# Optimization experiments

Hardware: AMD Instinct MI355X
Metric: run time of the kernel (lower is better)

## Reference

```python
import jax, jax.numpy as jnp
import numpy as np

S, L, D = 50, 1024, 768
D4 = D // 4

def _ln(x, g, b, eps=1e-5):
    m = jnp.mean(x, axis=-1, keepdims=True)
    v = jnp.mean((x - m) ** 2, axis=-1, keepdims=True)
    return (x - m) * jax.lax.rsqrt(v + eps) * g + b

def _attn(x, Wq, Wk, Wv):
    # x: [N, D]; low-rank q/k (D4), values are the raw input, then output proj Wv.
    q = x @ Wq                      # [N, D4]
    k = x @ Wk                      # [N, D4]
    u = (q @ k.T) / jnp.sqrt(jnp.float32(q.shape[-1]))
    a = jax.nn.softmax(u, axis=-1)  # [N, N]
    return (a @ x) @ Wv             # [N, D]

def setup_inputs() -> dict:
    key = jax.random.key(0)
    ks = jax.random.split(key, 16)
    g = lambda i, shape: jax.random.normal(ks[i], shape, dtype=jnp.float32) * 0.02
    return dict(
        x=jax.random.normal(ks[0], (S, L, D), dtype=jnp.float32),
        pre_Wq=g(1, (S, D, D4)), pre_Wk=g(2, (S, D, D4)), pre_Wv=g(3, (S, D, D)),
        ln1_g=jnp.ones((S, D)), ln1_b=jnp.zeros((S, D)),
        pre_W1=g(4, (S, D, D4)), pre_b1=jnp.zeros((S, D4)),
        pre_W2=g(5, (S, D4, D)), pre_b2=jnp.zeros((S, D)),
        ln4p_g=jnp.ones((S, D)), ln4p_b=jnp.zeros((S, D)),
        cross_Wq=g(6, (D, D4)), cross_Wk=g(7, (D, D4)), cross_Wv=g(8, (D, D)),
        ln2_g=jnp.ones((D,)), ln2_b=jnp.zeros((D,)),
        post_Wq=g(9, (S, D, D4)), post_Wk=g(10, (S, D, D4)), post_Wv=g(11, (S, D, D)),
        ln3_g=jnp.ones((S, D)), ln3_b=jnp.zeros((S, D)),
        post_W1=g(12, (S, D, D4)), post_b1=jnp.zeros((S, D4)),
        post_W2=g(13, (S, D4, D)), post_b2=jnp.zeros((S, D)),
        ln4_g=jnp.ones((S, D)), ln4_b=jnp.zeros((S, D)),
    )

def reference(x, pre_Wq, pre_Wk, pre_Wv, ln1_g, ln1_b,
              pre_W1, pre_b1, pre_W2, pre_b2, ln4p_g, ln4p_b,
              cross_Wq, cross_Wk, cross_Wv, ln2_g, ln2_b,
              post_Wq, post_Wk, post_Wv, ln3_g, ln3_b,
              post_W1, post_b1, post_W2, post_b2, ln4_g, ln4_b):
    # step_wise forward; dropout is identity at inference.
    # pre_self_step: per-step Attention (step dim vmapped == loop over n_step)
    h = jax.vmap(_attn)(x, pre_Wq, pre_Wk, pre_Wv)          # [S, L, D]
    x = jax.vmap(_ln)(x + h, ln1_g, ln1_b)
    # pre_mlp: per-step bottleneck MLP
    h = jax.nn.relu(jnp.einsum('sld,sdf->slf', x, pre_W1) + pre_b1[:, None, :])
    h = jnp.einsum('slf,sfd->sld', h, pre_W2) + pre_b2[:, None, :]
    x = jax.vmap(_ln)(x + h, ln4p_g, ln4p_b)
    # cross_step: shared Attention over the step axis (seq positions as batch)
    xt = jnp.transpose(x, (1, 0, 2))                        # [L, S, D]
    h = jax.vmap(_attn, in_axes=(0, None, None, None))(xt, cross_Wq, cross_Wk, cross_Wv)
    xt = _ln(xt + h, ln2_g, ln2_b)
    x = jnp.transpose(xt, (1, 0, 2))                        # [S, L, D]
    # post_self_step
    h = jax.vmap(_attn)(x, post_Wq, post_Wk, post_Wv)
    x = jax.vmap(_ln)(x + h, ln3_g, ln3_b)
    # post_mlp
    h = jax.nn.relu(jnp.einsum('sld,sdf->slf', x, post_W1) + post_b1[:, None, :])
    h = jnp.einsum('slf,sfd->sld', h, post_W2) + post_b2[:, None, :]
    x = jax.vmap(_ln)(x + h, ln4_g, ln4_b)
    return x
```

## Files before the change

### kernel.cpp

```cpp
#include <hip/hip_runtime.h>


typedef __bf16 bf16x8 __attribute__((ext_vector_type(8)));
typedef float f32x4 __attribute__((ext_vector_type(4)));

template<int BNN, int BF32>
__global__ __launch_bounds__(256) void gemm_k(
    const __bf16* __restrict__ A, const void* __restrict__ Bv, __bf16* __restrict__ C,
    int M, int N, int K, int Kb,
    int lda, int ldb, int ldc,
    long long sA, long long sB, long long sC,
    const float* __restrict__ bias, long long sBias, int relu)
{
    __shared__ __bf16 As[64][72];
    __shared__ __bf16 Bs[64][72];

    const int batch = blockIdx.z;
    A += (long long)batch * sA;
    C += (long long)batch * sC;

    const int m0 = blockIdx.x * 64;
    const int n0 = blockIdx.y * 64;
    const int tid = threadIdx.x;
    const int lane = tid & 63;
    const int wave = tid >> 6;
    const int wr = wave >> 1, wc = wave & 1;

    f32x4 acc[2][2];
    #pragma unroll
    for (int i = 0; i < 2; i++)
        #pragma unroll
        for (int j = 0; j < 2; j++)
            acc[i][j] = f32x4{0.f, 0.f, 0.f, 0.f};

    for (int kb = 0; kb < K; kb += 64) {
        {
            const int row = tid >> 2;
            const int cs = (tid & 3) << 4;
            const int gr = m0 + row;
            __bf16* dst = &As[row][cs];
            if (gr < M) {
                const __bf16* src = A + (long long)gr * lda + kb + cs;
                *(bf16x8*)dst       = *(const bf16x8*)src;
                *(bf16x8*)(dst + 8) = *(const bf16x8*)(src + 8);
            } else {
                #pragma unroll
                for (int i = 0; i < 16; i++) dst[i] = (__bf16)0.f;
            }
        }
        if (BNN) {
            const int kk = tid >> 2;
            const int ns = (tid & 3) << 4;
            const int gk = kb + kk;
            const bool kok = gk < Kb;
            if (BF32) {
                const float* src = (const float*)Bv + (long long)batch * sB
                                 + (long long)gk * ldb + n0 + ns;
                if (kok && (n0 + ns + 16 <= N)) {
                    #pragma unroll
                    for (int q = 0; q < 4; q++) {
                        float4 v = *(const float4*)(src + 4 * q);
                        Bs[ns + 4 * q + 0][kk] = (__bf16)v.x;
                        Bs[ns + 4 * q + 1][kk] = (__bf16)v.y;
                        Bs[ns + 4 * q + 2][kk] = (__bf16)v.z;
                        Bs[ns + 4 * q + 3][kk] = (__bf16)v.w;
                    }
                } else {
                    for (int i = 0; i < 16; i++) {
                        const int n = n0 + ns + i;
                        Bs[ns + i][kk] = (kok && n < N) ? (__bf16)src[i] : (__bf16)0.f;
                    }
                }
            } else {
                const __bf16* src = (const __bf16*)Bv + (long long)batch * sB
                                  + (long long)gk * ldb + n0 + ns;
                if (kok && (n0 + ns + 16 <= N)) {
                    bf16x8 v0 = *(const bf16x8*)src;
                    bf16x8 v1 = *(const bf16x8*)(src + 8);
                    #pragma unroll
                    for (int i = 0; i < 8; i++) Bs[ns + i][kk] = v0[i];
                    #pragma unroll
                    for (int i = 0; i < 8; i++) Bs[ns + 8 + i][kk] = v1[i];
                } else {
                    for (int i = 0; i < 16; i++) {
                        const int n = n0 + ns + i;
                        Bs[ns + i][kk] = (kok && n < N) ? src[i] : (__bf16)0.f;
                    }
                }
            }
        } else {
            const int row = tid >> 2;
            const int cs = (tid & 3) << 4;
            const int gn = n0 + row;
            __bf16* dst = &Bs[row][cs];
            if (gn < N) {
                const __bf16* src = (const __bf16*)Bv + (long long)batch * sB
                                  + (long long)gn * ldb + kb + cs;
                *(bf16x8*)dst       = *(const bf16x8*)src;
                *(bf16x8*)(dst + 8) = *(const bf16x8*)(src + 8);
            } else {
                #pragma unroll
                for (int i = 0; i < 16; i++) dst[i] = (__bf16)0.f;
            }
        }
        __syncthreads();

        #pragma unroll
        for (int ks = 0; ks < 64; ks += 32) {
            const int kf = ks + ((lane >> 4) << 3);
            bf16x8 av[2], bv[2];
            #pragma unroll
            for (int mi = 0; mi < 2; mi++)
                av[mi] = *(const bf16x8*)&As[wr * 32 + mi * 16 + (lane & 15)][kf];
            #pragma unroll
            for (int ni = 0; ni < 2; ni++)
                bv[ni] = *(const bf16x8*)&Bs[wc * 32 + ni * 16 + (lane & 15)][kf];
            #pragma unroll
            for (int mi = 0; mi < 2; mi++)
                #pragma unroll
                for (int ni = 0; ni < 2; ni++)
                    acc[mi][ni] = __builtin_amdgcn_mfma_f32_16x16x32_bf16(
                        av[mi], bv[ni], acc[mi][ni], 0, 0, 0);
        }
        __syncthreads();
    }

    const int rb = (lane >> 4) << 2;
    const int cc = lane & 15;
    #pragma unroll
    for (int mi = 0; mi < 2; mi++) {
        #pragma unroll
        for (int ni = 0; ni < 2; ni++) {
            const int col = n0 + wc * 32 + ni * 16 + cc;
            if (col >= N) continue;
            float bvl = 0.f;
            if (bias) bvl = bias[(long long)batch * sBias + col];
            #pragma unroll
            for (int r = 0; r < 4; r++) {
                const int row = m0 + wr * 32 + mi * 16 + rb + r;
                if (row < M) {
                    float v = acc[mi][ni][r] + bvl;
                    if (relu) v = fmaxf(v, 0.f);
                    C[(long long)row * ldc + col] = (__bf16)v;
                }
            }
        }
    }
}

__device__ __forceinline__ float wave_sum(float v) {
    #pragma unroll
    for (int o = 32; o > 0; o >>= 1) v += __shfl_xor(v, o);
    return v;
}
__device__ __forceinline__ float wave_max(float v) {
    #pragma unroll
    for (int o = 32; o > 0; o >>= 1) v = fmaxf(v, __shfl_xor(v, o));
    return v;
}

__global__ __launch_bounds__(256) void softmax_self_k(__bf16* __restrict__ u, float scale) {
    __shared__ float red[4];
    const long long row = blockIdx.x;
    __bf16* p = u + row * 1024;
    const int t = threadIdx.x;
    float v[4];
    float mx = -1e30f;
    #pragma unroll
    for (int i = 0; i < 4; i++) { v[i] = (float)p[t + i * 256]; mx = fmaxf(mx, v[i]); }
    mx = wave_max(mx);
    if ((t & 63) == 0) red[t >> 6] = mx;
    __syncthreads();
    mx = fmaxf(fmaxf(red[0], red[1]), fmaxf(red[2], red[3]));
    float s = 0.f;
    #pragma unroll
    for (int i = 0; i < 4; i++) { v[i] = __expf(scale * (v[i] - mx)); s += v[i]; }
    s = wave_sum(s);
    __syncthreads();
    if ((t & 63) == 0) red[t >> 6] = s;
    __syncthreads();
    s = red[0] + red[1] + red[2] + red[3];
    const float inv = 1.f / s;
    #pragma unroll
    for (int i = 0; i < 4; i++) p[t + i * 256] = (__bf16)(v[i] * inv);
}

__global__ __launch_bounds__(64) void softmax_cross_k(__bf16* __restrict__ u, float scale) {
    const long long row = blockIdx.x;
    __bf16* p = u + row * 64;
    const int lane = threadIdx.x;
    float v = (lane < 50) ? (float)p[lane] : -1e30f;
    float mx = wave_max(v);
    float e = (lane < 50) ? __expf(scale * (v - mx)) : 0.f;
    float s = wave_sum(e);
    p[lane] = (__bf16)(e / s);
}

__global__ __launch_bounds__(256) void add_ln_k(
    const __bf16* __restrict__ x, const __bf16* __restrict__ h, void* __restrict__ out,
    const float* __restrict__ g, const float* __restrict__ b, int mode, int outf32)
{
    __shared__ float red[4];
    const long long r = blockIdx.x;
    const __bf16* xr = x + r * 768;
    const __bf16* hr = h + r * 768;
    long long orow; const float *gp, *bp;
    if (mode == 0) {
        orow = r;
        const long long s = r >> 10;
        gp = g + s * 768; bp = b + s * 768;
    } else {
        const long long l = r / 50, s2 = r % 50;
        orow = s2 * 1024 + l;
        gp = g; bp = b;
    }
    const int t = threadIdx.x;
    float v[3]; float sum = 0.f;
    #pragma unroll
    for (int i = 0; i < 3; i++) { const int d = t + i * 256; v[i] = (float)xr[d] + (float)hr[d]; sum += v[i]; }
    sum = wave_sum(sum);
    if ((t & 63) == 0) red[t >> 6] = sum;
    __syncthreads();
    const float mean = (red[0] + red[1] + red[2] + red[3]) * (1.f / 768.f);
    float vs = 0.f;
    #pragma unroll
    for (int i = 0; i < 3; i++) { const float d = v[i] - mean; vs += d * d; }
    vs = wave_sum(vs);
    __syncthreads();
    if ((t & 63) == 0) red[t >> 6] = vs;
    __syncthreads();
    const float rstd = rsqrtf((red[0] + red[1] + red[2] + red[3]) * (1.f / 768.f) + 1e-5f);
    #pragma unroll
    for (int i = 0; i < 3; i++) {
        const int d = t + i * 256;
        const float o = (v[i] - mean) * rstd * gp[d] + bp[d];
        if (outf32) ((float*)out)[orow * 768 + d] = o;
        else        ((__bf16*)out)[orow * 768 + d] = (__bf16)o;
    }
}

__global__ __launch_bounds__(256) void transpose_sl_k(const __bf16* __restrict__ in,
                                                      __bf16* __restrict__ out) {
    const long long r = blockIdx.x;
    const long long s = r >> 10, l = r & 1023;
    const __bf16* ir = in + r * 768;
    __bf16* orow = out + (l * 50 + s) * 768;
    for (int i = threadIdx.x; i < 768; i += 256) orow[i] = ir[i];
}

__global__ __launch_bounds__(256) void cvt_f32_bf16_k(const float* __restrict__ in,
                                                      __bf16* __restrict__ out) {
    const long long i = ((long long)blockIdx.x * 256 + threadIdx.x) * 8;
    float4 a = *(const float4*)(in + i);
    float4 b = *(const float4*)(in + i + 4);
    bf16x8 o;
    o[0] = (__bf16)a.x; o[1] = (__bf16)a.y; o[2] = (__bf16)a.z; o[3] = (__bf16)a.w;
    o[4] = (__bf16)b.x; o[5] = (__bf16)b.y; o[6] = (__bf16)b.z; o[7] = (__bf16)b.w;
    *(bf16x8*)(out + i) = o;
}

extern "C" void kernel_launch(void* const* d_in, const int* in_sizes, int n_in,
                              void* d_out, int out_size, void* d_ws, size_t ws_size,
                              hipStream_t stream)
{
    const float SCALE = 0.07216878364870322f;
    auto inf = [&](int i) { return (const float*)d_in[i]; };

    char* w = (char*)d_ws;
    __bf16* xw = (__bf16*)(w + 0LL);
    __bf16* hw = (__bf16*)(w + 78643200LL);
    __bf16* tw = (__bf16*)(w + 157286400LL);
    __bf16* xt = (__bf16*)(w + 235929600LL);
    __bf16* qw = (__bf16*)(w + 314572800LL);
    __bf16* kw = (__bf16*)(w + 334233600LL);
    __bf16* G  = (__bf16*)(w + 353894400LL);
    if (ws_size < 458752000ULL) return;

    auto gemm_w = [&](const __bf16* A, const float* B, __bf16* C,
                      int M, int N, int K, int lda, int ldb, int ldc,
                      long long sA, long long sB, long long sC, int batch,
                      const float* bias, long long sBias, int relu) {
        dim3 grid((M + 63) / 64, (N + 63) / 64, batch);
        gemm_k<1, 1><<<grid, dim3(256), 0, stream>>>(A, B, C, M, N, K, K, lda, ldb, ldc,
                                                     sA, sB, sC, bias, sBias, relu);
    };
    auto gemm_a = [&](const __bf16* A, const __bf16* B, __bf16* C,
                      int M, int N, int K, int Kb, int lda, int ldb, int ldc,
                      long long sA, long long sB, long long sC, int batch) {
        dim3 grid((M + 63) / 64, (N + 63) / 64, batch);
        gemm_k<1, 0><<<grid, dim3(256), 0, stream>>>(A, B, C, M, N, K, Kb, lda, ldb, ldc,
                                                     sA, sB, sC, nullptr, 0, 0);
    };
    auto gemm_nt = [&](const __bf16* A, const __bf16* B, __bf16* C,
                       int M, int N, int K, int lda, int ldb, int ldc,
                       long long sA, long long sB, long long sC, int batch) {
        dim3 grid((M + 63) / 64, (N + 63) / 64, batch);
        gemm_k<0, 0><<<grid, dim3(256), 0, stream>>>(A, B, C, M, N, K, K, lda, ldb, ldc,
                                                     sA, sB, sC, nullptr, 0, 0);
    };

    cvt_f32_bf16_k<<<19200, 256, 0, stream>>>(inf(0), xw);

    auto self_attn = [&](const float* Wq, const float* Wk, const float* Wv,
                         const float* g, const float* b) {
        gemm_w(xw, Wq, qw, 1024, 192, 768, 768, 192, 192,
               786432LL, 147456LL, 196608LL, 50, nullptr, 0, 0);
        gemm_w(xw, Wk, kw, 1024, 192, 768, 768, 192, 192,
               786432LL, 147456LL, 196608LL, 50, nullptr, 0, 0);
        gemm_nt(qw, kw, G, 1024, 1024, 192, 192, 192, 1024,
                196608LL, 196608LL, 1048576LL, 50);
        softmax_self_k<<<51200, 256, 0, stream>>>(G, SCALE);
        gemm_a(G, xw, tw, 1024, 768, 1024, 1024, 1024, 768, 768,
               1048576LL, 786432LL, 786432LL, 50);
        gemm_w(tw, Wv, hw, 1024, 768, 768, 768, 768, 768,
               786432LL, 589824LL, 786432LL, 50, nullptr, 0, 0);
        add_ln_k<<<51200, 256, 0, stream>>>(xw, hw, xw, g, b, 0, 0);
    };
    auto mlp = [&](const float* W1, const float* b1, const float* W2, const float* b2,
                   const float* g, const float* b, void* outp, int outf32) {
        gemm_w(xw, W1, qw, 1024, 192, 768, 768, 192, 192,
               786432LL, 147456LL, 196608LL, 50, b1, 192LL, 1);
        gemm_w(qw, W2, hw, 1024, 768, 192, 192, 768, 768,
               196608LL, 147456LL, 786432LL, 50, b2, 768LL, 0);
        add_ln_k<<<51200, 256, 0, stream>>>(xw, hw, outp, g, b, 0, outf32);
    };

    self_attn(inf(1), inf(2), inf(3), inf(4), inf(5));
    mlp(inf(6), inf(7), inf(8), inf(9), inf(10), inf(11), xw, 0);

    transpose_sl_k<<<51200, 256, 0, stream>>>(xw, xt);
    gemm_w(xt, inf(12), qw, 51200, 192, 768, 768, 192, 192, 0, 0, 0, 1, nullptr, 0, 0);
    gemm_w(xt, inf(13), kw, 51200, 192, 768, 768, 192, 192, 0, 0, 0, 1, nullptr, 0, 0);
    gemm_nt(qw, kw, G, 50, 50, 192, 192, 192, 64, 9600LL, 9600LL, 3200LL, 1024);
    softmax_cross_k<<<51200, 64, 0, stream>>>(G, SCALE);
    gemm_a(G, xt, tw, 50, 768, 64, 50, 64, 768, 768,
           3200LL, 38400LL, 38400LL, 1024);
    gemm_w(tw, inf(14), hw, 51200, 768, 768, 768, 768, 768, 0, 0, 0, 1, nullptr, 0, 0);
    add_ln_k<<<51200, 256, 0, stream>>>(xt, hw, xw, inf(15), inf(16), 1, 0);

    self_attn(inf(17), inf(18), inf(19), inf(20), inf(21));
    mlp(inf(22), inf(23), inf(24), inf(25), inf(26), inf(27), d_out, 1);
}
```

Before: 2.890 ms.

## Add 128x128 direct-to-LDS MFMA GEMM with pre-transposed bf16 weights and vectorize elementwise kernels

Adds a new 128x128-tile GEMM that loads A and transposed B straight into swizzled LDS using global_load_lds and runs a 4x4 grid of MFMA 16x16x32 tiles per wave. Weights are first transposed and converted to bf16 by a tiled transpose kernel, and x is transposed for the attention-value GEMM, so every large matmul becomes an NT GEMM. Softmax, add+LayerNorm and the step/sequence transpose kernels now use vectorized loads and stores, and the cross softmax packs four rows per block. The cost is extra transpose launches and memory traffic per layer, and the new GEMM clamps out-of-range rows instead of zero-filling them and has no K-tail handling.

```diff
diff --git a/kernel.cpp b/kernel.cpp
--- a/kernel.cpp
+++ b/kernel.cpp
@@ -2,7 +2,142 @@
 
 
 typedef __bf16 bf16x8 __attribute__((ext_vector_type(8)));
+typedef __bf16 bf16x4 __attribute__((ext_vector_type(4)));
 typedef float f32x4 __attribute__((ext_vector_type(4)));
+
+typedef __attribute__((address_space(3))) void lds_t;
+typedef __attribute__((address_space(1))) const void gbl_t;
+
+__device__ __forceinline__ void gload16(const void* g, void* l) {
+    __builtin_amdgcn_global_load_lds((gbl_t*)g, (lds_t*)l, 16, 0, 0);
+}
+
+__global__ __launch_bounds__(256) void gemm128_k(
+    const __bf16* __restrict__ A, const __bf16* __restrict__ Bt, __bf16* __restrict__ C,
+    int M, int N, int K, int lda, int ldb, int ldc,
+    long long sA, long long sB, long long sC,
+    const float* __restrict__ bias, long long sBias, int relu)
+{
+    __shared__ __bf16 As[128 * 64];
+    __shared__ __bf16 Bs[128 * 64];
+
+    const int batch = blockIdx.z;
+    A  += (long long)batch * sA;
+    Bt += (long long)batch * sB;
+    C  += (long long)batch * sC;
+
+    const int m0 = blockIdx.x * 128;
+    const int n0 = blockIdx.y * 128;
+    const int tid  = threadIdx.x;
+    const int lane = tid & 63;
+    const int wave = tid >> 6;
+    const int wr = wave >> 1, wc = wave & 1;
+    const int l15 = lane & 15;
+
+    const __bf16* aSrc[4];
+    const __bf16* bSrc[4];
+    #pragma unroll
+    for (int r = 0; r < 4; r++) {
+        const int g   = r * 256 + tid;
+        const int row = g >> 3;
+        const int ch  = (g & 7) ^ (row & 7);
+        int ra = m0 + row; if (ra > M - 1) ra = M - 1;
+        int rb = n0 + row; if (rb > N - 1) rb = N - 1;
+        aSrc[r] = A  + (long long)ra * lda + (ch << 3);
+        bSrc[r] = Bt + (long long)rb * ldb + (ch << 3);
+    }
+    __bf16* aD = As + wave * 512;
+    __bf16* bD = Bs + wave * 512;
+
+    f32x4 acc[4][4];
+    #pragma unroll
+    for (int i = 0; i < 4; i++)
+        #pragma unroll
+        for (int j = 0; j < 4; j++) acc[i][j] = f32x4{0.f, 0.f, 0.f, 0.f};
+
+    for (int kb = 0; kb < K; kb += 64) {
+        #pragma unroll
+        for (int r = 0; r < 4; r++) gload16(aSrc[r] + kb, aD + r * 2048);
+        #pragma unroll
+        for (int r = 0; r < 4; r++) gload16(bSrc[r] + kb, bD + r * 2048);
+        __syncthreads();
+
+        #pragma unroll
+        for (int ks = 0; ks < 2; ks++) {
+            const int cg = ks * 4 + (lane >> 4);
+            const int so = ((cg ^ (l15 & 7)) << 3);
+            bf16x8 av[4], bv[4];
+            #pragma unroll
+            for (int mi = 0; mi < 4; mi++)
+                av[mi] = *(const bf16x8*)&As[(wr * 64 + mi * 16 + l15) * 64 + so];
+            #pragma unroll
+            for (int ni = 0; ni < 4; ni++)
+                bv[ni] = *(const bf16x8*)&Bs[(wc * 64 + ni * 16 + l15) * 64 + so];
+            #pragma unroll
+            for (int mi = 0; mi < 4; mi++)
+                #pragma unroll
+                for (int ni = 0; ni < 4; ni++)
+                    acc[mi][ni] = __builtin_amdgcn_mfma_f32_16x16x32_bf16(
+                        av[mi], bv[ni], acc[mi][ni], 0, 0, 0);
+        }
+        __syncthreads();
+    }
+
+    const int rb4 = (lane >> 4) << 2;
+    #pragma unroll
+    for (int mi = 0; mi < 4; mi++) {
+        #pragma unroll
+        for (int ni = 0; ni < 4; ni++) {
+            const int col = n0 + wc * 64 + ni * 16 + l15;
+            if (col >= N) continue;
+            float bvl = 0.f;
+            if (bias) bvl = bias[(long long)batch * sBias + col];
+            #pragma unroll
+            for (int r = 0; r < 4; r++) {
+                const int row = m0 + wr * 64 + mi * 16 + rb4 + r;
+                if (row < M) {
+                    float v = acc[mi][ni][r] + bvl;
+                    if (relu) v = fmaxf(v, 0.f);
+                    C[(long long)row * ldc + col] = (__bf16)v;
+                }
+            }
+        }
+    }
+}
+
+template<int INF32>
+__global__ __launch_bounds__(256) void trans_k(
+    const void* __restrict__ in, __bf16* __restrict__ out,
+    int R, int Cn, long long sIn, long long sOut)
+{
+    __shared__ float tile[32][33];
+    const int b  = blockIdx.z;
+    const int r0 = blockIdx.x * 32, c0 = blockIdx.y * 32;
+    const int t  = threadIdx.x;
+    {
+        const int rl = t >> 3;
+        const int cl = (t & 7) << 2;
+        const long long src = (long long)b * sIn + (long long)(r0 + rl) * Cn + c0 + cl;
+        if (INF32) {
+            float4 v = *(const float4*)((const float*)in + src);
+            tile[rl][cl + 0] = v.x; tile[rl][cl + 1] = v.y;
+            tile[rl][cl + 2] = v.z; tile[rl][cl + 3] = v.w;
+        } else {
+            bf16x4 v = *(const bf16x4*)((const __bf16*)in + src);
+            tile[rl][cl + 0] = (float)v[0]; tile[rl][cl + 1] = (float)v[1];
+            tile[rl][cl + 2] = (float)v[2]; tile[rl][cl + 3] = (float)v[3];
+        }
+    }
+    __syncthreads();
+    {
+        const int c2 = t >> 3;
+        const int r2 = (t & 7) << 2;
+        bf16x4 o;
+        o[0] = (__bf16)tile[r2 + 0][c2]; o[1] = (__bf16)tile[r2 + 1][c2];
+        o[2] = (__bf16)tile[r2 + 2][c2]; o[3] = (__bf16)tile[r2 + 3][c2];
+        *(bf16x4*)(out + (long long)b * sOut + (long long)(c0 + c2) * R + r0 + r2) = o;
+    }
+}
 
 template<int BNN, int BF32>
 __global__ __launch_bounds__(256) void gemm_k(
@@ -30,8 +165,7 @@
     #pragma unroll
     for (int i = 0; i < 2; i++)
         #pragma unroll
-        for (int j = 0; j < 2; j++)
-            acc[i][j] = f32x4{0.f, 0.f, 0.f, 0.f};
+        for (int j = 0; j < 2; j++) acc[i][j] = f32x4{0.f, 0.f, 0.f, 0.f};
 
     for (int kb = 0; kb < K; kb += 64) {
         {
@@ -53,39 +187,19 @@
             const int ns = (tid & 3) << 4;
             const int gk = kb + kk;
             const bool kok = gk < Kb;
-            if (BF32) {
-                const float* src = (const float*)Bv + (long long)batch * sB
-                                 + (long long)gk * ldb + n0 + ns;
-                if (kok && (n0 + ns + 16 <= N)) {
-                    #pragma unroll
-                    for (int q = 0; q < 4; q++) {
-                        float4 v = *(const float4*)(src + 4 * q);
-                        Bs[ns + 4 * q + 0][kk] = (__bf16)v.x;
-                        Bs[ns + 4 * q + 1][kk] = (__bf16)v.y;
-                        Bs[ns + 4 * q + 2][kk] = (__bf16)v.z;
-                        Bs[ns + 4 * q + 3][kk] = (__bf16)v.w;
-                    }
-                } else {
-                    for (int i = 0; i < 16; i++) {
-                        const int n = n0 + ns + i;
-                        Bs[ns + i][kk] = (kok && n < N) ? (__bf16)src[i] : (__bf16)0.f;
-                    }
-                }
+            const __bf16* src = (const __bf16*)Bv + (long long)batch * sB
+                              + (long long)gk * ldb + n0 + ns;
+            if (kok && (n0 + ns + 16 <= N)) {
+                bf16x8 v0 = *(const bf16x8*)src;
+                bf16x8 v1 = *(const bf16x8*)(src + 8);
+                #pragma unroll
+                for (int i = 0; i < 8; i++) Bs[ns + i][kk] = v0[i];
+                #pragma unroll
+                for (int i = 0; i < 8; i++) Bs[ns + 8 + i][kk] = v1[i];
             } else {
-                const __bf16* src = (const __bf16*)Bv + (long long)batch * sB
-                                  + (long long)gk * ldb + n0 + ns;
-                if (kok && (n0 + ns + 16 <= N)) {
-                    bf16x8 v0 = *(const bf16x8*)src;
-                    bf16x8 v1 = *(const bf16x8*)(src + 8);
-                    #pragma unroll
-                    for (int i = 0; i < 8; i++) Bs[ns + i][kk] = v0[i];
-                    #pragma unroll
-                    for (int i = 0; i < 8; i++) Bs[ns + 8 + i][kk] = v1[i];
-                } else {
-                    for (int i = 0; i < 16; i++) {
-                        const int n = n0 + ns + i;
-                        Bs[ns + i][kk] = (kok && n < N) ? src[i] : (__bf16)0.f;
-                    }
+                for (int i = 0; i < 16; i++) {
+                    const int n = n0 + ns + i;
+                    Bs[ns + i][kk] = (kok && n < N) ? src[i] : (__bf16)0.f;
                 }
             }
         } else {
@@ -164,10 +278,11 @@
     const long long row = blockIdx.x;
     __bf16* p = u + row * 1024;
     const int t = threadIdx.x;
+    bf16x4 raw = *(const bf16x4*)(p + t * 4);
     float v[4];
     float mx = -1e30f;
     #pragma unroll
-    for (int i = 0; i < 4; i++) { v[i] = (float)p[t + i * 256]; mx = fmaxf(mx, v[i]); }
+    for (int i = 0; i < 4; i++) { v[i] = (float)raw[i]; mx = fmaxf(mx, v[i]); }
     mx = wave_max(mx);
     if ((t & 63) == 0) red[t >> 6] = mx;
     __syncthreads();
@@ -181,14 +296,16 @@
     __syncthreads();
     s = red[0] + red[1] + red[2] + red[3];
     const float inv = 1.f / s;
-    #pragma unroll
-    for (int i = 0; i < 4; i++) p[t + i * 256] = (__bf16)(v[i] * inv);
-}
-
-__global__ __launch_bounds__(64) void softmax_cross_k(__bf16* __restrict__ u, float scale) {
-    const long long row = blockIdx.x;
+    bf16x4 o;
+    #pragma unroll
+    for (int i = 0; i < 4; i++) o[i] = (__bf16)(v[i] * inv);
+    *(bf16x4*)(p + t * 4) = o;
+}
+
+__global__ __launch_bounds__(256) void softmax_cross_k(__bf16* __restrict__ u, float scale) {
+    const long long row = (long long)blockIdx.x * 4 + (threadIdx.x >> 6);
     __bf16* p = u + row * 64;
-    const int lane = threadIdx.x;
+    const int lane = threadIdx.x & 63;
     float v = (lane < 50) ? (float)p[lane] : -1e30f;
     float mx = wave_max(v);
     float e = (lane < 50) ? __expf(scale * (v - mx)) : 0.f;
@@ -196,11 +313,11 @@
     p[lane] = (__bf16)(e / s);
 }
 
-__global__ __launch_bounds__(256) void add_ln_k(
+__global__ __launch_bounds__(192) void add_ln_k(
     const __bf16* __restrict__ x, const __bf16* __restrict__ h, void* __restrict__ out,
     const float* __restrict__ g, const float* __restrict__ b, int mode, int outf32)
 {
-    __shared__ float red[4];
+    __shared__ float red[3];
     const long long r = blockIdx.x;
     const __bf16* xr = x + r * 768;
     const __bf16* hr = h + r * 768;
@@ -215,37 +332,46 @@
         gp = g; bp = b;
     }
     const int t = threadIdx.x;
-    float v[3]; float sum = 0.f;
-    #pragma unroll
-    for (int i = 0; i < 3; i++) { const int d = t + i * 256; v[i] = (float)xr[d] + (float)hr[d]; sum += v[i]; }
+    const int d = t * 4;
+    bf16x4 xv = *(const bf16x4*)(xr + d);
+    bf16x4 hv = *(const bf16x4*)(hr + d);
+    float v[4]; float sum = 0.f;
+    #pragma unroll
+    for (int i = 0; i < 4; i++) { v[i] = (float)xv[i] + (float)hv[i]; sum += v[i]; }
     sum = wave_sum(sum);
     if ((t & 63) == 0) red[t >> 6] = sum;
     __syncthreads();
-    const float mean = (red[0] + red[1] + red[2] + red[3]) * (1.f / 768.f);
+    const float mean = (red[0] + red[1] + red[2]) * (1.f / 768.f);
     float vs = 0.f;
     #pragma unroll
-    for (int i = 0; i < 3; i++) { const float d = v[i] - mean; vs += d * d; }
+    for (int i = 0; i < 4; i++) { const float dd = v[i] - mean; vs += dd * dd; }
     vs = wave_sum(vs);
     __syncthreads();
     if ((t & 63) == 0) red[t >> 6] = vs;
     __syncthreads();
-    const float rstd = rsqrtf((red[0] + red[1] + red[2] + red[3]) * (1.f / 768.f) + 1e-5f);
-    #pragma unroll
-    for (int i = 0; i < 3; i++) {
-        const int d = t + i * 256;
-        const float o = (v[i] - mean) * rstd * gp[d] + bp[d];
-        if (outf32) ((float*)out)[orow * 768 + d] = o;
-        else        ((__bf16*)out)[orow * 768 + d] = (__bf16)o;
-    }
-}
-
-__global__ __launch_bounds__(256) void transpose_sl_k(const __bf16* __restrict__ in,
+    const float rstd = rsqrtf((red[0] + red[1] + red[2]) * (1.f / 768.f) + 1e-5f);
+    float4 gv = *(const float4*)(gp + d);
+    float4 bv = *(const float4*)(bp + d);
+    const float o0 = (v[0] - mean) * rstd * gv.x + bv.x;
+    const float o1 = (v[1] - mean) * rstd * gv.y + bv.y;
+    const float o2 = (v[2] - mean) * rstd * gv.z + bv.z;
+    const float o3 = (v[3] - mean) * rstd * gv.w + bv.w;
+    if (outf32) {
+        float4 o{o0, o1, o2, o3};
+        *(float4*)((float*)out + orow * 768 + d) = o;
+    } else {
+        bf16x4 o;
+        o[0] = (__bf16)o0; o[1] = (__bf16)o1; o[2] = (__bf16)o2; o[3] = (__bf16)o3;
+        *(bf16x4*)((__bf16*)out + orow * 768 + d) = o;
+    }
+}
+
+__global__ __launch_bounds__(192) void transpose_sl_k(const __bf16* __restrict__ in,
                                                       __bf16* __restrict__ out) {
-    const long long r = blockIdx.x;
+    const long long r = (long long)blockIdx.x * 2 + (threadIdx.x >= 96);
+    const int c = (threadIdx.x % 96) * 8;
     const long long s = r >> 10, l = r & 1023;
-    const __bf16* ir = in + r * 768;
-    __bf16* orow = out + (l * 50 + s) * 768;
-    for (int i = threadIdx.x; i < 768; i += 256) orow[i] = ir[i];
+    *(bf16x8*)(out + (l * 50 + s) * 768 + c) = *(const bf16x8*)(in + r * 768 + c);
 }
 
 __global__ __launch_bounds__(256) void cvt_f32_bf16_k(const float* __restrict__ in,
@@ -274,69 +400,83 @@
     __bf16* qw = (__bf16*)(w + 314572800LL);
     __bf16* kw = (__bf16*)(w + 334233600LL);
     __bf16* G  = (__bf16*)(w + 353894400LL);
+    __bf16* wa = G;
     if (ws_size < 458752000ULL) return;
 
-    auto gemm_w = [&](const __bf16* A, const float* B, __bf16* C,
-                      int M, int N, int K, int lda, int ldb, int ldc,
-                      long long sA, long long sB, long long sC, int batch,
-                      const float* bias, long long sBias, int relu) {
-        dim3 grid((M + 63) / 64, (N + 63) / 64, batch);
-        gemm_k<1, 1><<<grid, dim3(256), 0, stream>>>(A, B, C, M, N, K, K, lda, ldb, ldc,
-                                                     sA, sB, sC, bias, sBias, relu);
+    auto g128 = [&](const __bf16* A, const __bf16* Bt, __bf16* C,
+                    int M, int N, int K, int lda, int ldb, int ldc,
+                    long long sA, long long sB, long long sC, int batch,
+                    const float* bias, long long sBias, int relu) {
+        dim3 grid((M + 127) / 128, (N + 127) / 128, batch);
+        gemm128_k<<<grid, dim3(256), 0, stream>>>(A, Bt, C, M, N, K, lda, ldb, ldc,
+                                                  sA, sB, sC, bias, sBias, relu);
     };
-    auto gemm_a = [&](const __bf16* A, const __bf16* B, __bf16* C,
-                      int M, int N, int K, int Kb, int lda, int ldb, int ldc,
-                      long long sA, long long sB, long long sC, int batch) {
-        dim3 grid((M + 63) / 64, (N + 63) / 64, batch);
-        gemm_k<1, 0><<<grid, dim3(256), 0, stream>>>(A, B, C, M, N, K, Kb, lda, ldb, ldc,
-                                                     sA, sB, sC, nullptr, 0, 0);
-    };
-    auto gemm_nt = [&](const __bf16* A, const __bf16* B, __bf16* C,
-                       int M, int N, int K, int lda, int ldb, int ldc,
-                       long long sA, long long sB, long long sC, int batch) {
-        dim3 grid((M + 63) / 64, (N + 63) / 64, batch);
-        gemm_k<0, 0><<<grid, dim3(256), 0, stream>>>(A, B, C, M, N, K, K, lda, ldb, ldc,
-                                                     sA, sB, sC, nullptr, 0, 0);
+    auto transw = [&](const float* W, __bf16* outp, int R, int Cn, int batch) {
+        dim3 grid(R / 32, Cn / 32, batch);
+        trans_k<1><<<grid, dim3(256), 0, stream>>>(W, outp, R, Cn,
+                                                   (long long)R * Cn, (long long)R * Cn);
     };
 
     cvt_f32_bf16_k<<<19200, 256, 0, stream>>>(inf(0), xw);
 
     auto self_attn = [&](const float* Wq, const float* Wk, const float* Wv,
                          const float* g, const float* b) {
-        gemm_w(xw, Wq, qw, 1024, 192, 768, 768, 192, 192,
-               786432LL, 147456LL, 196608LL, 50, nullptr, 0, 0);
-        gemm_w(xw, Wk, kw, 1024, 192, 768, 768, 192, 192,
-               786432LL, 147456LL, 196608LL, 50, nullptr, 0, 0);
-        gemm_nt(qw, kw, G, 1024, 1024, 192, 192, 192, 1024,
-                196608LL, 196608LL, 1048576LL, 50);
+        transw(Wq, wa, 768, 192, 50);
+        g128(xw, wa, qw, 1024, 192, 768, 768, 768, 192,
+             786432LL, 147456LL, 196608LL, 50, nullptr, 0, 0);
+        transw(Wk, wa, 768, 192, 50);
+        g128(xw, wa, kw, 1024, 192, 768, 768, 768, 192,
+             786432LL, 147456LL, 196608LL, 50, nullptr, 0, 0);
+        g128(qw, kw, G, 1024, 1024, 192, 192, 192, 1024,
+             196608LL, 196608LL, 1048576LL, 50, nullptr, 0, 0);
         softmax_self_k<<<51200, 256, 0, stream>>>(G, SCALE);
-        gemm_a(G, xw, tw, 1024, 768, 1024, 1024, 1024, 768, 768,
-               1048576LL, 786432LL, 786432LL, 50);
-        gemm_w(tw, Wv, hw, 1024, 768, 768, 768, 768, 768,
-               786432LL, 589824LL, 786432LL, 50, nullptr, 0, 0);
-        add_ln_k<<<51200, 256, 0, stream>>>(xw, hw, xw, g, b, 0, 0);
+        {
+            dim3 grid(32, 24, 50);
+            trans_k<0><<<grid, dim3(256), 0, stream>>>(xw, hw, 1024, 768,
+                                                       786432LL, 786432LL);
+        }
+        g128(G, hw, tw, 1024, 768, 1024, 1024, 1024, 768,
+             1048576LL, 786432LL, 786432LL, 50, nullptr, 0, 0);
+        transw(Wv, wa, 768, 768, 50);
+        g128(tw, wa, hw, 1024, 768, 768, 768, 768, 768,
+             786432LL, 589824LL, 786432LL, 50, nullptr, 0, 0);
+        add_ln_k<<<51200, 192, 0, stream>>>(xw, hw, xw, g, b, 0, 0);
     };
     auto mlp = [&](const float* W1, const float* b1, const float* W2, const float* b2,
                    const float* g, const float* b, void* outp, int outf32) {
-        gemm_w(xw, W1, qw, 1024, 192, 768, 768, 192, 192,
-               786432LL, 147456LL, 196608LL, 50, b1, 192LL, 1);
-        gemm_w(qw, W2, hw, 1024, 768, 192, 192, 768, 768,
-               196608LL, 147456LL, 786432LL, 50, b2, 768LL, 0);
-        add_ln_k<<<51200, 256, 0, stream>>>(xw, hw, outp, g, b, 0, outf32);
+        transw(W1, wa, 768, 192, 50);
+        g128(xw, wa, qw, 1024, 192, 768, 768, 768, 192,
+             786432LL, 147456LL, 196608LL, 50, b1, 192LL, 1);
+        transw(W2, wa, 192, 768, 50);
+        g128(qw, wa, hw, 1024, 768, 192, 192, 192, 768,
+             196608LL, 147456LL, 786432LL, 50, b2, 768LL, 0);
+        add_ln_k<<<51200, 192, 0, stream>>>(xw, hw, outp, g, b, 0, outf32);
     };
 
     self_attn(inf(1), inf(2), inf(3), inf(4), inf(5));
     mlp(inf(6), inf(7), inf(8), inf(9), inf(10), inf(11), xw, 0);
 
-    transpose_sl_k<<<51200, 256, 0, stream>>>(xw, xt);
-    gemm_w(xt, inf(12), qw, 51200, 192, 768, 768, 192, 192, 0, 0, 0, 1, nullptr, 0, 0);
-    gemm_w(xt, inf(13), kw, 51200, 192, 768, 768, 192, 192, 0, 0, 0, 1, nullptr, 0, 0);
-    gemm_nt(qw, kw, G, 50, 50, 192, 192, 192, 64, 9600LL, 9600LL, 3200LL, 1024);
-    softmax_cross_k<<<51200, 64, 0, stream>>>(G, SCALE);
-    gemm_a(G, xt, tw, 50, 768, 64, 50, 64, 768, 768,
-           3200LL, 38400LL, 38400LL, 1024);
-    gemm_w(tw, inf(14), hw, 51200, 768, 768, 768, 768, 768, 0, 0, 0, 1, nullptr, 0, 0);
-    add_ln_k<<<51200, 256, 0, stream>>>(xt, hw, xw, inf(15), inf(16), 1, 0);
+    transpose_sl_k<<<25600, 192, 0, stream>>>(xw, xt);
+    transw(inf(12), wa, 768, 192, 1);
+    g128(xt, wa, qw, 51200, 192, 768, 768, 768, 192, 0, 0, 0, 1, nullptr, 0, 0);
+    transw(inf(13), wa, 768, 192, 1);
+    g128(xt, wa, kw, 51200, 192, 768, 768, 768, 192, 0, 0, 0, 1, nullptr, 0, 0);
+    {
+        dim3 grid(1, 1, 1024);
+        gemm_k<0, 0><<<grid, dim3(256), 0, stream>>>(qw, kw, G, 50, 50, 192, 192,
+                                                     192, 192, 64, 9600LL, 9600LL,
+                                                     3200LL, nullptr, 0, 0);
+    }
+    softmax_cross_k<<<12800, 256, 0, stream>>>(G, SCALE);
+    {
+        dim3 grid(1, 12, 1024);
+        gemm_k<1, 0><<<grid, dim3(256), 0, stream>>>(G, xt, tw, 50, 768, 64, 50,
+                                                     64, 768, 768, 3200LL, 38400LL,
+                                                     38400LL, nullptr, 0, 0);
+    }
+    transw(inf(14), qw, 768, 768, 1);
+    g128(tw, qw, hw, 51200, 768, 768, 768, 768, 768, 0, 0, 0, 1, nullptr, 0, 0);
+    add_ln_k<<<51200, 192, 0, stream>>>(xt, hw, xw, inf(15), inf(16), 1, 0);
 
     self_attn(inf(17), inf(18), inf(19), inf(20), inf(21));
     mlp(inf(22), inf(23), inf(24), inf(25), inf(26), inf(27), d_out, 1);
```

After: 2.548 ms. 1.13x faster.
